# Optimization experiments

Measured on AMD Instinct MI355X. Metric: run time of the kernel, lower is better.

The kernel has to match this reference:

```python
import jax, jax.numpy as jnp
import numpy as np

D_MODEL = 1024
D_STATE = 128
D_CONV = 4
EXPAND = 2
HEADDIM = 64
D_INNER = EXPAND * D_MODEL          # 2048
NHEADS = D_INNER // HEADDIM          # 32
CONV_CH = D_INNER + 2 * D_STATE      # conv acts on x, B, C (ngroups=1)
D_IN_PROJ = 2 * D_INNER + 2 * D_STATE + NHEADS
CHUNK = 128


def setup_inputs() -> dict:
    key = jax.random.key(0)
    ks = jax.random.split(key, 8)
    B, L = 4, 2048
    return {
        'x': jax.random.normal(ks[0], (B, L, D_MODEL), jnp.float32),
        'ln_w': jnp.ones((D_MODEL,), jnp.float32),
        'ln_b': jnp.zeros((D_MODEL,), jnp.float32),
        'in_proj_w': jax.random.normal(ks[1], (D_IN_PROJ, D_MODEL), jnp.float32) * 0.02,
        'conv_w': jax.random.normal(ks[2], (CONV_CH, D_CONV), jnp.float32) * 0.2,
        'conv_b': jnp.zeros((CONV_CH,), jnp.float32),
        'dt_bias': jax.random.normal(ks[3], (NHEADS,), jnp.float32) * 0.5,
        'A_log': jax.random.uniform(ks[4], (NHEADS,), jnp.float32, 0.0, 1.5),
        'D': jax.random.normal(ks[5], (NHEADS,), jnp.float32) * 0.1 + 1.0,
        'norm_w': jnp.ones((D_INNER,), jnp.float32),
        'out_proj_w': jax.random.normal(ks[6], (D_MODEL, D_INNER), jnp.float32) * 0.02,
    }


def segsum(a):
    # a: (..., T) -> (..., T, T) with out[i, j] = sum_{j < k <= i} a[k], -inf above diag
    T = a.shape[-1]
    a_rep = jnp.broadcast_to(a[..., :, None], a.shape + (T,))
    a_masked = jnp.where(jnp.tril(jnp.ones((T, T), bool), -1), a_rep, 0.0)
    seg = jnp.cumsum(a_masked, axis=-2)
    return jnp.where(jnp.tril(jnp.ones((T, T), bool), 0), seg, -jnp.inf)


def _ssd(X, a, Bm, Cm):
    # Chunked SSD (Mamba2). X: (b,l,h,p) pre-multiplied by dt; a: (b,l,h)=dt*A; Bm,Cm: (b,l,n)
    b, l, h, p = X.shape
    c = l // CHUNK
    Xc = X.reshape(b, c, CHUNK, h, p)
    Bc = Bm.reshape(b, c, CHUNK, -1)
    Cc = Cm.reshape(b, c, CHUNK, -1)
    ac = a.reshape(b, c, CHUNK, h).transpose(0, 3, 1, 2)   # (b,h,c,q)
    a_cs = jnp.cumsum(ac, axis=-1)                          # (b,h,c,q)
    Lm = jnp.exp(segsum(ac))                                # (b,h,c,q,q)
    # intra-chunk (diagonal) part
    Y_diag = jnp.einsum('bcln,bcsn,bhcls,bcshp->bclhp', Cc, Bc, Lm, Xc)
    # chunk final states
    decay_states = jnp.exp(a_cs[..., -1:] - a_cs)           # (b,h,c,q)
    states = jnp.einsum('bcln,bhcl,bclhp->bchpn', Bc, decay_states, Xc)
    states = jnp.concatenate([jnp.zeros_like(states[:, :1]), states], axis=1)  # (b,c+1,h,p,n)
    a_chunk = jnp.pad(a_cs[..., -1], ((0, 0), (0, 0), (1, 0)))  # (b,h,c+1)
    decay_chunk = jnp.exp(segsum(a_chunk))                  # (b,h,c+1,c+1)
    prev_states = jnp.einsum('bhzc,bchpn->bzhpn', decay_chunk, states)[:, :-1]  # (b,c,h,p,n)
    # inter-chunk (off-diagonal) part
    Y_off = jnp.einsum('bcln,bchpn,bhcl->bclhp', Cc, prev_states, jnp.exp(a_cs))
    return (Y_diag + Y_off).reshape(b, l, h, p)


def reference(x, ln_w, ln_b, in_proj_w, conv_w, conv_b, dt_bias, A_log, D, norm_w, out_proj_w):
    B, L, _ = x.shape
    # pre-LayerNorm
    mu = x.mean(-1, keepdims=True)
    var = ((x - mu) ** 2).mean(-1, keepdims=True)
    h = (x - mu) / jnp.sqrt(var + 1e-5) * ln_w + ln_b
    # Mamba2 in_proj -> [z, xBC, dt]
    zxbcdt = h @ in_proj_w.T
    z = zxbcdt[..., :D_INNER]
    xBC = zxbcdt[..., D_INNER:D_INNER + CONV_CH]
    dt = jax.nn.softplus(zxbcdt[..., -NHEADS:] + dt_bias)  # (B,L,H)
    # causal depthwise conv1d + SiLU
    xp = jnp.pad(xBC, ((0, 0), (D_CONV - 1, 0), (0, 0)))
    conv = sum(xp[:, k:k + L, :] * conv_w[:, k] for k in range(D_CONV)) + conv_b
    xBC = jax.nn.silu(conv)
    xs = xBC[..., :D_INNER].reshape(B, L, NHEADS, HEADDIM)
    Bm = xBC[..., D_INNER:D_INNER + D_STATE]
    Cm = xBC[..., D_INNER + D_STATE:]
    A = -jnp.exp(A_log)                                    # (H,)
    Y = _ssd(xs * dt[..., None], dt * A, Bm, Cm)
    Y = Y + D[None, None, :, None] * xs                    # D skip connection
    y = Y.reshape(B, L, D_INNER)
    # gated RMSNorm (norm_before_gate=False)
    y = y * jax.nn.silu(z)
    y = y * jax.lax.rsqrt(jnp.mean(y * y, -1, keepdims=True) + 1e-5) * norm_w
    out = y @ out_proj_w.T
    # dropout in eval mode = identity; residual
    return out + x
```

## Files before the change

### kernel.cpp

```cpp
#include <hip/hip_runtime.h>
#include <math.h>

#define BATCH   4
#define LSEQ    2048
#define DMODEL  1024
#define DSTATE  128
#define HEADDIM 64
#define DINNER  2048
#define NHEADS  32
#define CONVCH  2304
#define DINPROJ 4384
#define NPAD    4608
#define CHUNKL  128
#define NCHUNK  16
#define ROWS    (BATCH*LSEQ)

#define B_Z     ((size_t)0)
#define B_XBC   (B_Z   + (size_t)ROWS*DINNER*2)
#define B_DT    (B_XBC + (size_t)ROWS*CONVCH*2)
#define B_XS    (B_DT  + (size_t)ROWS*NHEADS*4)
#define B_BC    (B_XS  + (size_t)ROWS*DINNER*2)
#define B_Y     (B_BC  + (size_t)ROWS*256*2)
#define B_ASUM  (B_Y   + (size_t)ROWS*DINNER*2)
#define B_END   (B_ASUM + (size_t)BATCH*NCHUNK*NHEADS*4)

typedef __attribute__((ext_vector_type(8))) short bf16x8;
typedef __attribute__((ext_vector_type(4))) float f32x4;

__device__ __forceinline__ float b2f(ushort u) {
  union { uint32_t i; float f; } v; v.i = ((uint32_t)u) << 16; return v.f;
}
__device__ __forceinline__ ushort f2b(float f) {
  union { float f; uint32_t i; } v; v.f = f;
  uint32_t r = (v.i + 0x7FFFu + ((v.i >> 16) & 1u)) >> 16;
  return (ushort)r;
}

__device__ __forceinline__ void async_ld16(const void* g, void* l) {
  __builtin_amdgcn_global_load_lds(
      (const __attribute__((address_space(1))) unsigned int*)g,
      (__attribute__((address_space(3))) unsigned int*)l, 16, 0, 0);
}


template<int K>
__device__ __forceinline__ void stage256(const ushort* __restrict__ A,
    const ushort* __restrict__ W, int m0, int n0, int tid, int t,
    ushort* lA, ushort* lB)
{
  const int k0 = t * 64;
  #pragma unroll
  for (int it = 0; it < 4; it++) {
    int s = it*512 + tid;
    int row = s >> 3;
    int g = (s & 7) ^ (row & 7);
    async_ld16(A + (size_t)(m0 + row)*K + k0 + g*8, lA + (size_t)s*8);
  }
  #pragma unroll
  for (int it = 0; it < 4; it++) {
    int s = it*512 + tid;
    int row = s >> 3;
    int g = (s & 7) ^ (row & 7);
    async_ld16(W + (size_t)(n0 + row)*K + k0 + g*8, lB + (size_t)s*8);
  }
}

__device__ __forceinline__ void compute256(const ushort* lA, const ushort* lB,
    int wr, int wc, int rl, int q, f32x4 acc[8][4])
{
  #pragma unroll
  for (int kh = 0; kh < 2; kh++) {
    bf16x8 af[8], bfr[4];
    #pragma unroll
    for (int i = 0; i < 8; i++) {
      int row = wr*128 + i*16 + rl;
      af[i] = *(const bf16x8*)&lA[(size_t)(row*8 + ((kh*4 + q) ^ (row & 7)))*8];
    }
    #pragma unroll
    for (int j = 0; j < 4; j++) {
      int row = wc*64 + j*16 + rl;
      bfr[j] = *(const bf16x8*)&lB[(size_t)(row*8 + ((kh*4 + q) ^ (row & 7)))*8];
    }
    #pragma unroll
    for (int i = 0; i < 8; i++)
      #pragma unroll
      for (int j = 0; j < 4; j++)
        acc[i][j] = __builtin_amdgcn_mfma_f32_16x16x32_bf16(af[i], bfr[j], acc[i][j], 0, 0, 0);
  }
}

template<int K>
__device__ __forceinline__ void stage_tile(const ushort* __restrict__ A,
    const ushort* __restrict__ W, int m0, int n0, int tid, int t,
    ushort* lA, ushort* lB)
{
  const int k0 = t * 64;
  #pragma unroll
  for (int it = 0; it < 4; it++) {
    int s = it*512 + tid;
    int row = s >> 3;
    int g = (s & 7) ^ (row & 7);
    async_ld16(A + (size_t)(m0 + row)*K + k0 + g*8, lA + (size_t)s*8);
  }
  #pragma unroll
  for (int it = 0; it < 2; it++) {
    int s = it*512 + tid;
    int row = s >> 3;
    int g = (s & 7) ^ (row & 7);
    async_ld16(W + (size_t)(n0 + row)*K + k0 + g*8, lB + (size_t)s*8);
  }
}

__device__ __forceinline__ void compute_tile(const ushort* lA, const ushort* lB,
    int wr, int wc, int rl, int q, f32x4 acc[4][4])
{
  #pragma unroll
  for (int kh = 0; kh < 2; kh++) {
    bf16x8 af[4], bfr[4];
    #pragma unroll
    for (int i = 0; i < 4; i++) {
      int row = wr*64 + i*16 + rl;
      af[i] = *(const bf16x8*)&lA[(size_t)(row*8 + ((kh*4 + q) ^ (row & 7)))*8];
    }
    #pragma unroll
    for (int j = 0; j < 4; j++) {
      int row = wc*64 + j*16 + rl;
      bfr[j] = *(const bf16x8*)&lB[(size_t)(row*8 + ((kh*4 + q) ^ (row & 7)))*8];
    }
    #pragma unroll
    for (int i = 0; i < 4; i++)
      #pragma unroll
      for (int j = 0; j < 4; j++)
        acc[i][j] = __builtin_amdgcn_mfma_f32_16x16x32_bf16(af[i], bfr[j], acc[i][j], 0, 0, 0);
  }
}

__global__ __launch_bounds__(256) void convert_win_kernel(const float* __restrict__ W,
                                                          ushort* __restrict__ Wb)
{
  size_t i = (size_t)blockIdx.x*256 + threadIdx.x;
  Wb[i] = (i < (size_t)DINPROJ*DMODEL) ? f2b(W[i]) : (ushort)0;
}

__global__ __launch_bounds__(256) void convert_wout_kernel(const float* __restrict__ W,
                                                           ushort* __restrict__ Wb)
{
  size_t i = (size_t)blockIdx.x*256 + threadIdx.x;
  Wb[i] = f2b(W[i]);
}

__global__ __launch_bounds__(256) void ln_kernel(const float* __restrict__ x,
    const float* __restrict__ w, const float* __restrict__ bias, ushort* __restrict__ h)
{
  const int row = blockIdx.x;
  const int t = threadIdx.x;
  const float* xr = x + (size_t)row * DMODEL;
  float v[4];
  float s = 0.f;
  #pragma unroll
  for (int i = 0; i < 4; i++) { v[i] = xr[t + i*256]; s += v[i]; }
  __shared__ float red[4];
  #pragma unroll
  for (int o = 32; o > 0; o >>= 1) s += __shfl_down(s, o, 64);
  if ((t & 63) == 0) red[t >> 6] = s;
  __syncthreads();
  float mean = (red[0]+red[1]+red[2]+red[3]) * (1.f/DMODEL);
  float vs = 0.f;
  #pragma unroll
  for (int i = 0; i < 4; i++) { float d = v[i]-mean; vs += d*d; }
  #pragma unroll
  for (int o = 32; o > 0; o >>= 1) vs += __shfl_down(vs, o, 64);
  __syncthreads();
  if ((t & 63) == 0) red[t >> 6] = vs;
  __syncthreads();
  float rstd = rsqrtf((red[0]+red[1]+red[2]+red[3]) * (1.f/DMODEL) + 1e-5f);
  ushort* hr = h + (size_t)row * DMODEL;
  #pragma unroll
  for (int i = 0; i < 4; i++) {
    int c = t + i*256;
    hr[c] = f2b((v[i]-mean)*rstd*w[c] + bias[c]);
  }
}

__global__ __launch_bounds__(512, 1) void gemm_inproj_256(const ushort* __restrict__ A,
    const ushort* __restrict__ W, ushort* __restrict__ z, ushort* __restrict__ xbc,
    float* __restrict__ dtr, const float* __restrict__ dtb)
{
  __shared__ ushort smem[65536];
  const int tid = threadIdx.x;
  const int lane = tid & 63;
  const int w = tid >> 6;
  const int wr = w >> 2;
  const int wc = w & 3;
  const int rl = lane & 15;
  const int q  = lane >> 4;

  const int orig = blockIdx.x;
  const int xcd  = orig & 7;
  const int jj   = orig >> 3;
  const int m0 = (xcd*4 + jj/18) * 256;
  const int n0 = (jj % 18) * 256;

  f32x4 acc[8][4];
  #pragma unroll
  for (int i = 0; i < 8; i++)
    #pragma unroll
    for (int j = 0; j < 4; j++) acc[i][j] = (f32x4)(0.f);

  constexpr int NT = DMODEL / 64;
  stage256<DMODEL>(A, W, m0, n0, tid, 0, smem, smem + 16384);
  for (int t = 0; t < NT; t++) {
    const ushort* cA = smem + (t & 1)*32768;
    const ushort* cB = cA + 16384;
    if (t + 1 < NT) {
      ushort* nA = smem + ((t+1) & 1)*32768;
      stage256<DMODEL>(A, W, m0, n0, tid, t + 1, nA, nA + 16384);
      asm volatile("s_waitcnt vmcnt(8)" ::: "memory");
    } else {
      asm volatile("s_waitcnt vmcnt(0)" ::: "memory");
    }
    __builtin_amdgcn_s_barrier();
    __builtin_amdgcn_sched_barrier(0);
    __builtin_amdgcn_s_setprio(1);
    compute256(cA, cB, wr, wc, rl, q, acc);
    __builtin_amdgcn_s_setprio(0);
    __builtin_amdgcn_sched_barrier(0);
    __builtin_amdgcn_s_barrier();
  }

  const int colL = lane & 15;
  const int rowQ = (lane >> 4) * 4;
  if (n0 < DINNER + CONVCH) {
    #pragma unroll
    for (int i = 0; i < 8; i++)
      #pragma unroll
      for (int j = 0; j < 4; j++) {
        int col = wc*64 + j*16 + colL;
        int g = col >> 3;
        #pragma unroll
        for (int r = 0; r < 4; r++) {
          int row = wr*128 + i*16 + rowQ + r;
          int p = (g & 24) | ((g ^ row) & 7);
          smem[row*256 + p*8 + (col & 7)] = f2b(acc[i][j][r]);
        }
      }
    __syncthreads();
    ushort* outp; int coff, ncols;
    if (n0 < DINNER) { outp = z;   coff = n0;          ncols = DINNER; }
    else             { outp = xbc; coff = n0 - DINNER; ncols = CONVCH; }
    #pragma unroll
    for (int it = 0; it < 16; it++) {
      int idx = tid + it*512;
      int row = idx >> 5, g = idx & 31;
      int p = (g & 24) | ((g ^ row) & 7);
      *(uint4*)(outp + (size_t)(m0 + row)*ncols + coff + g*8) =
          *(const uint4*)&smem[row*256 + p*8];
    }
  } else {
    if (wc == 0) {
      #pragma unroll
      for (int i = 0; i < 8; i++)
        #pragma unroll
        for (int j = 0; j < 2; j++) {
          int lc = j*16 + colL;
          float bb = dtb[lc];
          #pragma unroll
          for (int r = 0; r < 4; r++) {
            float v = acc[i][j][r] + bb;
            v = (v > 20.f) ? v : log1pf(expf(v));
            dtr[(size_t)(m0 + wr*128 + i*16 + rowQ + r)*NHEADS + lc] = v;
          }
        }
    }
  }
}

__global__ __launch_bounds__(512, 1) void gemm_outproj_big(const ushort* __restrict__ A,
    const ushort* __restrict__ W, const float* __restrict__ x, float* __restrict__ out)
{
  __shared__ ushort smem[49152];
  ushort* lA0 = smem;
  ushort* lB0 = smem + 32768;
  float* fbuf = (float*)smem;
  const int tid = threadIdx.x;
  const int lane = tid & 63;
  const int w = tid >> 6;
  const int wr = w >> 1;
  const int wc = w & 1;
  const int rl = lane & 15;
  const int q  = lane >> 4;

  const int orig = blockIdx.x;
  const int xcd  = orig & 7;
  const int jj   = orig >> 3;
  const int m0 = (xcd*4 + (jj >> 3)) * 256;
  const int n0 = (jj & 7) * 128;

  f32x4 acc[4][4];
  #pragma unroll
  for (int i = 0; i < 4; i++)
    #pragma unroll
    for (int j = 0; j < 4; j++) acc[i][j] = (f32x4)(0.f);

  constexpr int NT = DINNER / 64;
  stage_tile<DINNER>(A, W, m0, n0, tid, 0, lA0, lB0);
  for (int t = 0; t < NT; t++) {
    const ushort* cA = lA0 + (size_t)(t & 1) * 16384;
    const ushort* cB = lB0 + (size_t)(t & 1) * 8192;
    if (t + 1 < NT) {
      stage_tile<DINNER>(A, W, m0, n0, tid, t + 1,
                         lA0 + (size_t)((t+1) & 1) * 16384,
                         lB0 + (size_t)((t+1) & 1) * 8192);
      asm volatile("s_waitcnt vmcnt(6)" ::: "memory");
    } else {
      asm volatile("s_waitcnt vmcnt(0)" ::: "memory");
    }
    __builtin_amdgcn_s_barrier();
    __builtin_amdgcn_sched_barrier(0);
    __builtin_amdgcn_s_setprio(1);
    compute_tile(cA, cB, wr, wc, rl, q, acc);
    __builtin_amdgcn_s_setprio(0);
    __builtin_amdgcn_sched_barrier(0);
    __builtin_amdgcn_s_barrier();
  }

  const int colL = lane & 15;
  const int rowQ = (lane >> 4) * 4;
  #pragma unroll
  for (int h = 0; h < 2; h++) {
    __syncthreads();
    if ((wr >> 1) == h) {
      #pragma unroll
      for (int i = 0; i < 4; i++)
        #pragma unroll
        for (int j = 0; j < 4; j++) {
          int col = wc*64 + j*16 + colL;
          int g = col >> 2;
          #pragma unroll
          for (int r = 0; r < 4; r++) {
            int row = (wr & 1)*64 + i*16 + rowQ + r;
            fbuf[row*128 + ((g ^ (row & 7)) << 2) + (col & 3)] = acc[i][j][r];
          }
        }
    }
    __syncthreads();
    #pragma unroll
    for (int it = 0; it < 8; it++) {
      int idx = tid + it*512;
      int row = idx >> 5, c4 = idx & 31;
      int gm = m0 + h*128 + row;
      float4 xv = *(const float4*)(x + (size_t)gm*DMODEL + n0 + c4*4);
      float4 vv = *(const float4*)&fbuf[row*128 + ((c4 ^ (row & 7)) << 2)];
      vv.x += xv.x; vv.y += xv.y; vv.z += xv.z; vv.w += xv.w;
      *(float4*)(out + (size_t)gm*DMODEL + n0 + c4*4) = vv;
    }
  }
}

__global__ __launch_bounds__(256) void conv_tiled(const ushort* __restrict__ xbc,
    const float* __restrict__ cw, const float* __restrict__ cb,
    ushort* __restrict__ xs, ushort* __restrict__ bcb)
{
  __shared__ ushort tile[35*256];
  const int tid = threadIdx.x;
  const int ch0 = blockIdx.x * 256;
  const int row0 = blockIdx.y * 32;
  const int l0 = row0 & (LSEQ-1);
  for (int idx = tid; idx < 35*32; idx += 256) {
    int r = idx >> 5, c16 = idx & 31;
    uint4 v = make_uint4(0,0,0,0);
    if (l0 + r - 3 >= 0)
      v = *(const uint4*)(xbc + (size_t)(row0 + r - 3)*CONVCH + ch0 + c16*8);
    *(uint4*)&tile[r*256 + c16*8] = v;
  }
  __syncthreads();
  const int ch = ch0 + tid;
  const float w0 = cw[ch*4+0], w1 = cw[ch*4+1], w2 = cw[ch*4+2], w3 = cw[ch*4+3];
  const float bias = cb[ch];
  const bool isX = (ch0 < DINNER);
  #pragma unroll 4
  for (int r = 0; r < 32; r++) {
    float acc = bias;
    acc = fmaf(b2f(tile[(r+0)*256 + tid]), w0, acc);
    acc = fmaf(b2f(tile[(r+1)*256 + tid]), w1, acc);
    acc = fmaf(b2f(tile[(r+2)*256 + tid]), w2, acc);
    acc = fmaf(b2f(tile[(r+3)*256 + tid]), w3, acc);
    float v = acc / (1.f + expf(-acc));
    if (isX) xs[(size_t)(row0 + r)*DINNER + ch] = f2b(v);
    else     bcb[(size_t)(row0 + r)*256 + (ch - DINNER)] = f2b(v);
  }
}

__global__ __launch_bounds__(256) void states_mfma(
    const ushort* __restrict__ xs, const ushort* __restrict__ bcb, const float* __restrict__ dt,
    const float* __restrict__ A_log, ushort* __restrict__ S, float* __restrict__ asum)
{
  constexpr int LDP = 136;
  __shared__ ushort lBT[128*LDP];
  __shared__ ushort lXT[64*LDP];
  __shared__ float dts[CHUNKL], acs[CHUNKL];
  __shared__ float wtot;
  const int hh = blockIdx.x, c = blockIdx.y, b = blockIdx.z;
  const int tid = threadIdx.x;
  const int lane = tid & 63;
  const int w = tid >> 6;
  const int rbase = b*LSEQ + c*CHUNKL;
  const size_t sbase = (size_t)((b*NCHUNK + c)*NHEADS + hh) * 8192;

  float pre = 0.f;
  if (tid < 128) {
    float myv = dt[(size_t)(rbase + tid)*NHEADS + hh];
    dts[tid] = myv;
    pre = myv;
    #pragma unroll
    for (int o = 1; o < 64; o <<= 1) {
      float u = __shfl_up(pre, o, 64);
      if ((tid & 63) >= o) pre += u;
    }
    if (tid == 63) wtot = pre;
  }
  #pragma unroll
  for (int it = 0; it < 8; it++) {
    int chunk = tid + it*256;
    int l = chunk >> 4, n8 = chunk & 15;
    ushort tmp[8];
    *(uint4*)tmp = *(const uint4*)(bcb + (size_t)(rbase + l)*256 + n8*8);
    #pragma unroll
    for (int u = 0; u < 8; u++) lBT[(n8*8+u)*LDP + l] = tmp[u];
  }
  __syncthreads();
  float alast_loc = 0.f;
  if (tid < 128) {
    float Aval = -expf(A_log[hh]);
    float a = (pre + ((tid >= 64) ? wtot : 0.f)) * Aval;
    acs[tid] = a;
    if (tid == 127) { asum[(b*NCHUNK + c)*NHEADS + hh] = a; }
  }
  __syncthreads();
  alast_loc = acs[CHUNKL-1];
  #pragma unroll
  for (int it = 0; it < 4; it++) {
    int chunk = tid + it*256;
    int l = chunk >> 3, p8 = (chunk & 7)*8;
    ushort tmp[8];
    *(uint4*)tmp = *(const uint4*)(xs + (size_t)(rbase + l)*DINNER + hh*HEADDIM + p8);
    float wl = dts[l] * expf(alast_loc - acs[l]);
    #pragma unroll
    for (int u = 0; u < 8; u++) lXT[(p8+u)*LDP + l] = f2b(b2f(tmp[u]) * wl);
  }
  __syncthreads();

  const int rl = lane & 15;
  const int kq = (lane >> 4) * 8;
  const int nb = w * 32;
  f32x4 acc[4][2];
  #pragma unroll
  for (int i = 0; i < 4; i++) { acc[i][0] = (f32x4)(0.f); acc[i][1] = (f32x4)(0.f); }
  #pragma unroll
  for (int k0 = 0; k0 < 128; k0 += 32) {
    bf16x8 af[4], bfr[2];
    #pragma unroll
    for (int i = 0; i < 4; i++) af[i]  = *(const bf16x8*)&lXT[(i*16 + rl)*LDP + k0 + kq];
    #pragma unroll
    for (int j = 0; j < 2; j++) bfr[j] = *(const bf16x8*)&lBT[(nb + j*16 + rl)*LDP + k0 + kq];
    #pragma unroll
    for (int i = 0; i < 4; i++)
      #pragma unroll
      for (int j = 0; j < 2; j++)
        acc[i][j] = __builtin_amdgcn_mfma_f32_16x16x32_bf16(af[i], bfr[j], acc[i][j], 0, 0, 0);
  }
  __syncthreads();
  const int colL = lane & 15;
  const int rowQ = (lane >> 4) * 4;
  #pragma unroll
  for (int i = 0; i < 4; i++)
    #pragma unroll
    for (int j = 0; j < 2; j++)
      #pragma unroll
      for (int r = 0; r < 4; r++)
        lXT[(i*16 + rowQ + r)*LDP + nb + j*16 + colL] = f2b(acc[i][j][r]);
  __syncthreads();
  #pragma unroll
  for (int it = 0; it < 4; it++) {
    int idx = tid + it*256;
    int row = idx >> 4, c8 = idx & 15;
    *(uint4*)(S + sbase + row*128 + c8*8) = *(const uint4*)&lXT[row*LDP + c8*8];
  }
}

__global__ __launch_bounds__(256) void scan_kernel(ushort* __restrict__ S, const float* __restrict__ asum)
{
  const int hh = blockIdx.x, sl = blockIdx.y, b = blockIdx.z;
  const int base0 = sl*2048 + threadIdx.x;
  float carry[8];
  #pragma unroll
  for (int i = 0; i < 8; i++) carry[i] = 0.f;
  for (int c = 0; c < NCHUNK; c++) {
    ushort* Sp = S + (size_t)((b*NCHUNK + c)*NHEADS + hh) * 8192;
    float dec = expf(asum[(b*NCHUNK + c)*NHEADS + hh]);
    #pragma unroll
    for (int i = 0; i < 8; i++) {
      int idx = base0 + i*256;
      float sv = b2f(Sp[idx]);
      Sp[idx] = f2b(carry[i]);
      carry[i] = fmaf(dec, carry[i], sv);
    }
  }
}

__global__ __launch_bounds__(256) void yssd_mfma(
    const ushort* __restrict__ xs, const ushort* __restrict__ bcb, const float* __restrict__ dt,
    const float* __restrict__ A_log, const float* __restrict__ Dvec,
    const ushort* __restrict__ S, ushort* __restrict__ y)
{
  constexpr int LDP = 136;
  __shared__ ushort lM [128*LDP];
  __shared__ ushort lXT[64*LDP];
  __shared__ float dts[CHUNKL], acs[CHUNKL];
  __shared__ float wtot;
  const int hh = blockIdx.x, c = blockIdx.y, b = blockIdx.z;
  const int tid = threadIdx.x;
  const int lane = tid & 63;
  const int w = tid >> 6;
  const int rbase = b*LSEQ + c*CHUNKL;
  const size_t sbase = (size_t)((b*NCHUNK + c)*NHEADS + hh) * 8192;
  const ushort* Bg = bcb + (size_t)rbase*256;
  const ushort* Cg = Bg + 128;

  #pragma unroll
  for (int it = 0; it < 4; it++) {
    int chunk = tid + it*256;
    int s = chunk >> 3, p0 = (chunk & 7)*8;
    ushort tmp[8];
    *(uint4*)tmp = *(const uint4*)(xs + (size_t)(rbase + s)*DINNER + hh*HEADDIM + p0);
    #pragma unroll
    for (int u = 0; u < 8; u++) lXT[(p0+u)*LDP + s] = tmp[u];
  }
  float pre = 0.f;
  if (tid < 128) {
    float myv = dt[(size_t)(rbase + tid)*NHEADS + hh];
    dts[tid] = myv;
    pre = myv;
    #pragma unroll
    for (int o = 1; o < 64; o <<= 1) {
      float u = __shfl_up(pre, o, 64);
      if ((tid & 63) >= o) pre += u;
    }
    if (tid == 63) wtot = pre;
  }
  __syncthreads();
  if (tid < 128) {
    float Aval = -expf(A_log[hh]);
    acs[tid] = (pre + ((tid >= 64) ? wtot : 0.f)) * Aval;
  }

  const int rl = lane & 15;
  const int kq = (lane >> 4) * 8;
  const int colL = lane & 15;
  const int rowQ = (lane >> 4) * 4;

  const int wm = (w & 1) * 64;
  const int wn = (w >> 1) * 64;
  f32x4 G[4][4];
  #pragma unroll
  for (int i = 0; i < 4; i++)
    #pragma unroll
    for (int j = 0; j < 4; j++) G[i][j] = (f32x4)(0.f);
  #pragma unroll
  for (int k0 = 0; k0 < 128; k0 += 32) {
    bf16x8 af[4], bfr[4];
    #pragma unroll
    for (int i = 0; i < 4; i++) af[i]  = *(const bf16x8*)(Cg + (size_t)(wm + i*16 + rl)*256 + k0 + kq);
    #pragma unroll
    for (int j = 0; j < 4; j++) bfr[j] = *(const bf16x8*)(Bg + (size_t)(wn + j*16 + rl)*256 + k0 + kq);
    #pragma unroll
    for (int i = 0; i < 4; i++)
      #pragma unroll
      for (int j = 0; j < 4; j++)
        G[i][j] = __builtin_amdgcn_mfma_f32_16x16x32_bf16(af[i], bfr[j], G[i][j], 0, 0, 0);
  }
  __syncthreads();

  #pragma unroll
  for (int j = 0; j < 4; j++) {
    int sIdx = wn + j*16 + colL;
    float as = acs[sIdx];
    float ds = dts[sIdx];
    #pragma unroll
    for (int i = 0; i < 4; i++) {
      #pragma unroll
      for (int r = 0; r < 4; r++) {
        int lIdx = wm + i*16 + rowQ + r;
        float m = (lIdx >= sIdx) ? G[i][j][r] * expf(acs[lIdx] - as) * ds : 0.f;
        lM[lIdx*LDP + sIdx] = f2b(m);
      }
    }
  }

  const int om = w * 32;
  f32x4 Y[2][4];
  #pragma unroll
  for (int i = 0; i < 2; i++)
    #pragma unroll
    for (int j = 0; j < 4; j++) Y[i][j] = (f32x4)(0.f);
  #pragma unroll
  for (int k0 = 0; k0 < 128; k0 += 32) {
    bf16x8 a2[2], b2[4];
    #pragma unroll
    for (int i = 0; i < 2; i++) a2[i] = *(const bf16x8*)(Cg + (size_t)(om + i*16 + rl)*256 + k0 + kq);
    #pragma unroll
    for (int j = 0; j < 4; j++) b2[j] = *(const bf16x8*)(S + sbase + (size_t)(j*16 + rl)*128 + k0 + kq);
    #pragma unroll
    for (int i = 0; i < 2; i++)
      #pragma unroll
      for (int j = 0; j < 4; j++)
        Y[i][j] = __builtin_amdgcn_mfma_f32_16x16x32_bf16(a2[i], b2[j], Y[i][j], 0, 0, 0);
  }
  #pragma unroll
  for (int i = 0; i < 2; i++)
    #pragma unroll
    for (int r = 0; r < 4; r++) {
      float e = expf(acs[om + i*16 + rowQ + r]);
      #pragma unroll
      for (int j = 0; j < 4; j++) Y[i][j][r] *= e;
    }
  __syncthreads();

  #pragma unroll
  for (int k0 = 0; k0 < 128; k0 += 32) {
    bf16x8 a3[2], b3[4];
    #pragma unroll
    for (int i = 0; i < 2; i++) a3[i] = *(const bf16x8*)&lM[(om + i*16 + rl)*LDP + k0 + kq];
    #pragma unroll
    for (int j = 0; j < 4; j++) b3[j] = *(const bf16x8*)&lXT[(j*16 + rl)*LDP + k0 + kq];
    #pragma unroll
    for (int i = 0; i < 2; i++)
      #pragma unroll
      for (int j = 0; j < 4; j++)
        Y[i][j] = __builtin_amdgcn_mfma_f32_16x16x32_bf16(a3[i], b3[j], Y[i][j], 0, 0, 0);
  }

  const float Dh = Dvec[hh];
  #pragma unroll
  for (int i = 0; i < 2; i++) {
    #pragma unroll
    for (int r = 0; r < 4; r++) {
      int lIdx = om + i*16 + rowQ + r;
      ushort* yrow = y + (size_t)(rbase + lIdx)*DINNER + hh*HEADDIM;
      #pragma unroll
      for (int j = 0; j < 4; j++) {
        int p = j*16 + colL;
        float val = Y[i][j][r] + Dh * b2f(lXT[p*LDP + lIdx]);
        yrow[p] = f2b(val);
      }
    }
  }
}

__global__ __launch_bounds__(256) void rmsnorm_kernel(ushort* __restrict__ y,
    const ushort* __restrict__ z, const float* __restrict__ nw)
{
  const int row = blockIdx.x;
  const int t = threadIdx.x;
  ushort* yr = y + (size_t)row*DINNER;
  const ushort* zr = z + (size_t)row*DINNER;
  float v[8];
  float ss = 0.f;
  #pragma unroll
  for (int i = 0; i < 8; i++) {
    int c = t + i*256;
    float zz = b2f(zr[c]);
    float g = b2f(yr[c]) * (zz / (1.f + expf(-zz)));
    v[i] = g;
    ss += g*g;
  }
  #pragma unroll
  for (int o = 32; o > 0; o >>= 1) ss += __shfl_down(ss, o, 64);
  __shared__ float red[4];
  if ((t & 63) == 0) red[t >> 6] = ss;
  __syncthreads();
  float scale = rsqrtf((red[0]+red[1]+red[2]+red[3]) * (1.f/DINNER) + 1e-5f);
  #pragma unroll
  for (int i = 0; i < 8; i++) {
    int c = t + i*256;
    yr[c] = f2b(v[i]*scale*nw[c]);
  }
}

extern "C" void kernel_launch(void* const* d_in, const int* in_sizes, int n_in,
                              void* d_out, int out_size, void* d_ws, size_t ws_size,
                              hipStream_t stream)
{
  const float* x    = (const float*)d_in[0];
  const float* lnw  = (const float*)d_in[1];
  const float* lnb  = (const float*)d_in[2];
  const float* win  = (const float*)d_in[3];
  const float* cw   = (const float*)d_in[4];
  const float* cb   = (const float*)d_in[5];
  const float* dtb  = (const float*)d_in[6];
  const float* alog = (const float*)d_in[7];
  const float* dvec = (const float*)d_in[8];
  const float* nw   = (const float*)d_in[9];
  const float* wout = (const float*)d_in[10];
  float* out = (float*)d_out;
  char* ws = (char*)d_ws;
  (void)in_sizes; (void)n_in; (void)out_size;

  if (ws_size < B_END) return;

  ushort* zb   = (ushort*)(ws + B_Z);
  ushort* xbcb = (ushort*)(ws + B_XBC);
  float*  dtr  = (float*) (ws + B_DT);
  ushort* xsb  = (ushort*)(ws + B_XS);
  ushort* bcb  = (ushort*)(ws + B_BC);
  ushort* yb   = (ushort*)(ws + B_Y);
  float*  asum = (float*) (ws + B_ASUM);
  ushort* Sb   = xbcb;
  ushort* hb   = yb;
  ushort* winB = (ushort*)(ws + B_Y + (size_t)ROWS*DMODEL*2);
  ushort* woutB= (ushort*)(ws + B_XBC + (size_t)BATCH*NCHUNK*NHEADS*HEADDIM*DSTATE*2);

  hipLaunchKernelGGL(convert_win_kernel, dim3((NPAD*DMODEL)/256), dim3(256), 0, stream, win, winB);
  hipLaunchKernelGGL(ln_kernel, dim3(ROWS), dim3(256), 0, stream, x, lnw, lnb, hb);
  hipLaunchKernelGGL(gemm_inproj_256, dim3(576), dim3(512), 0, stream, hb, winB, zb, xbcb, dtr, dtb);
  hipLaunchKernelGGL(conv_tiled, dim3(9, ROWS/32), dim3(256), 0, stream, xbcb, cw, cb, xsb, bcb);
  hipLaunchKernelGGL(convert_wout_kernel, dim3((DMODEL*DINNER)/256), dim3(256), 0, stream, wout, woutB);
  hipLaunchKernelGGL(states_mfma, dim3(NHEADS, NCHUNK, BATCH), dim3(256), 0, stream,
                     xsb, bcb, dtr, alog, Sb, asum);
  hipLaunchKernelGGL(scan_kernel, dim3(NHEADS, 4, BATCH), dim3(256), 0, stream, Sb, asum);
  hipLaunchKernelGGL(yssd_mfma, dim3(NHEADS, NCHUNK, BATCH), dim3(256), 0, stream,
                     xsb, bcb, dtr, alog, dvec, Sb, yb);
  hipLaunchKernelGGL(rmsnorm_kernel, dim3(ROWS), dim3(256), 0, stream, yb, zb, nw);
  hipLaunchKernelGGL(gemm_outproj_big, dim3(256), dim3(512), 0, stream, yb, woutB, x, out);
}
```

Baseline: 473.3 us.

## Restructure in_proj GEMM into quadrant phases with finer-grained async staging

The in_proj 256x256 GEMM main loop is rewritten so each K-step is split into four quadrant phases (2x2 sub-tiles of 128x128), each with its own barrier and MFMA burst. Half-tile global-to-LDS loads are interleaved between phases, with explicit vmcnt waits, so memory traffic overlaps compute at finer granularity than whole-tile double buffering. The warp layout changes to 2x4 with per-quadrant accumulators, and A fragments are reused across the two N quadrants. It adds more barriers per K-step, and the hand-tuned vmcnt counts risk races if they are wrong.

```diff
diff --git a/kernel.cpp b/kernel.cpp
--- a/kernel.cpp
+++ b/kernel.cpp
@@ -42,9 +42,61 @@
       (__attribute__((address_space(3))) unsigned int*)l, 16, 0, 0);
 }
 
+#define VMG(n) asm volatile("s_waitcnt vmcnt(" #n ")" ::: "memory")
+
 
 template<int K>
-__device__ __forceinline__ void stage256(const ushort* __restrict__ A,
+__device__ __forceinline__ void stage_half(const ushort* __restrict__ M,
+    int row0, int k0, int tid, ushort* dst)
+{
+  #pragma unroll
+  for (int it = 0; it < 2; it++) {
+    int s = it*512 + tid;
+    int rl = s >> 3;
+    int g = (s & 7) ^ (rl & 7);
+    async_ld16(M + (size_t)(row0 + rl)*K + k0 + g*8, dst + (size_t)s*8);
+  }
+}
+
+template<int QM, int QN, bool RDA>
+__device__ __forceinline__ void qphase(const ushort* __restrict__ bA,
+    const ushort* __restrict__ bB, int wq, int wn, int rl, int q,
+    bf16x8 (&af)[2][4], bf16x8 (&bfr)[2][2], f32x4 (&acc)[2][2][4][2])
+{
+  __builtin_amdgcn_s_barrier();
+  __builtin_amdgcn_sched_barrier(0);
+  if (RDA) {
+    #pragma unroll
+    for (int kh = 0; kh < 2; kh++)
+      #pragma unroll
+      for (int ii = 0; ii < 4; ii++) {
+        int row = QM*128 + wq*64 + ii*16 + rl;
+        af[kh][ii] = *(const bf16x8*)&bA[(size_t)(row*8 + ((kh*4 + q) ^ (row & 7)))*8];
+      }
+  }
+  #pragma unroll
+  for (int kh = 0; kh < 2; kh++)
+    #pragma unroll
+    for (int jj = 0; jj < 2; jj++) {
+      int row = QN*128 + wn*32 + jj*16 + rl;
+      bfr[kh][jj] = *(const bf16x8*)&bB[(size_t)(row*8 + ((kh*4 + q) ^ (row & 7)))*8];
+    }
+  __builtin_amdgcn_s_setprio(1);
+  #pragma unroll
+  for (int kh = 0; kh < 2; kh++)
+    #pragma unroll
+    for (int ii = 0; ii < 4; ii++)
+      #pragma unroll
+      for (int jj = 0; jj < 2; jj++)
+        acc[QM][QN][ii][jj] = __builtin_amdgcn_mfma_f32_16x16x32_bf16(
+            af[kh][ii], bfr[kh][jj], acc[QM][QN][ii][jj], 0, 0, 0);
+  __builtin_amdgcn_s_setprio(0);
+  __builtin_amdgcn_sched_barrier(0);
+  __builtin_amdgcn_s_barrier();
+}
+
+template<int K>
+__device__ __forceinline__ void stage_tile(const ushort* __restrict__ A,
     const ushort* __restrict__ W, int m0, int n0, int tid, int t,
     ushort* lA, ushort* lB)
 {
@@ -57,52 +109,6 @@
     async_ld16(A + (size_t)(m0 + row)*K + k0 + g*8, lA + (size_t)s*8);
   }
   #pragma unroll
-  for (int it = 0; it < 4; it++) {
-    int s = it*512 + tid;
-    int row = s >> 3;
-    int g = (s & 7) ^ (row & 7);
-    async_ld16(W + (size_t)(n0 + row)*K + k0 + g*8, lB + (size_t)s*8);
-  }
-}
-
-__device__ __forceinline__ void compute256(const ushort* lA, const ushort* lB,
-    int wr, int wc, int rl, int q, f32x4 acc[8][4])
-{
-  #pragma unroll
-  for (int kh = 0; kh < 2; kh++) {
-    bf16x8 af[8], bfr[4];
-    #pragma unroll
-    for (int i = 0; i < 8; i++) {
-      int row = wr*128 + i*16 + rl;
-      af[i] = *(const bf16x8*)&lA[(size_t)(row*8 + ((kh*4 + q) ^ (row & 7)))*8];
-    }
-    #pragma unroll
-    for (int j = 0; j < 4; j++) {
-      int row = wc*64 + j*16 + rl;
-      bfr[j] = *(const bf16x8*)&lB[(size_t)(row*8 + ((kh*4 + q) ^ (row & 7)))*8];
-    }
-    #pragma unroll
-    for (int i = 0; i < 8; i++)
-      #pragma unroll
-      for (int j = 0; j < 4; j++)
-        acc[i][j] = __builtin_amdgcn_mfma_f32_16x16x32_bf16(af[i], bfr[j], acc[i][j], 0, 0, 0);
-  }
-}
-
-template<int K>
-__device__ __forceinline__ void stage_tile(const ushort* __restrict__ A,
-    const ushort* __restrict__ W, int m0, int n0, int tid, int t,
-    ushort* lA, ushort* lB)
-{
-  const int k0 = t * 64;
-  #pragma unroll
-  for (int it = 0; it < 4; it++) {
-    int s = it*512 + tid;
-    int row = s >> 3;
-    int g = (s & 7) ^ (row & 7);
-    async_ld16(A + (size_t)(m0 + row)*K + k0 + g*8, lA + (size_t)s*8);
-  }
-  #pragma unroll
   for (int it = 0; it < 2; it++) {
     int s = it*512 + tid;
     int row = s >> 3;
@@ -182,7 +188,7 @@
   }
 }
 
-__global__ __launch_bounds__(512, 1) void gemm_inproj_256(const ushort* __restrict__ A,
+__global__ __launch_bounds__(512, 1) void gemm_inproj_8ph(const ushort* __restrict__ A,
     const ushort* __restrict__ W, ushort* __restrict__ z, ushort* __restrict__ xbc,
     float* __restrict__ dtr, const float* __restrict__ dtb)
 {
@@ -190,60 +196,112 @@
   const int tid = threadIdx.x;
   const int lane = tid & 63;
   const int w = tid >> 6;
-  const int wr = w >> 2;
-  const int wc = w & 3;
+  const int wq = w >> 2;
+  const int wn = w & 3;
   const int rl = lane & 15;
   const int q  = lane >> 4;
 
   const int orig = blockIdx.x;
   const int xcd  = orig & 7;
-  const int jj   = orig >> 3;
-  const int m0 = (xcd*4 + jj/18) * 256;
-  const int n0 = (jj % 18) * 256;
-
-  f32x4 acc[8][4];
-  #pragma unroll
-  for (int i = 0; i < 8; i++)
-    #pragma unroll
-    for (int j = 0; j < 4; j++) acc[i][j] = (f32x4)(0.f);
-
+  const int jj_  = orig >> 3;
+  const int m0 = (xcd*4 + jj_/18) * 256;
+  const int n0 = (jj_ % 18) * 256;
+
+  f32x4 acc[2][2][4][2];
+  #pragma unroll
+  for (int a = 0; a < 2; a++)
+    #pragma unroll
+    for (int b = 0; b < 2; b++)
+      #pragma unroll
+      for (int c = 0; c < 4; c++)
+        #pragma unroll
+        for (int d = 0; d < 2; d++) acc[a][b][c][d] = (f32x4)(0.f);
+
+  bf16x8 af[2][4], bfr[2][2];
   constexpr int NT = DMODEL / 64;
-  stage256<DMODEL>(A, W, m0, n0, tid, 0, smem, smem + 16384);
-  for (int t = 0; t < NT; t++) {
-    const ushort* cA = smem + (t & 1)*32768;
-    const ushort* cB = cA + 16384;
-    if (t + 1 < NT) {
-      ushort* nA = smem + ((t+1) & 1)*32768;
-      stage256<DMODEL>(A, W, m0, n0, tid, t + 1, nA, nA + 16384);
-      asm volatile("s_waitcnt vmcnt(8)" ::: "memory");
-    } else {
-      asm volatile("s_waitcnt vmcnt(0)" ::: "memory");
-    }
-    __builtin_amdgcn_s_barrier();
-    __builtin_amdgcn_sched_barrier(0);
-    __builtin_amdgcn_s_setprio(1);
-    compute256(cA, cB, wr, wc, rl, q, acc);
-    __builtin_amdgcn_s_setprio(0);
-    __builtin_amdgcn_sched_barrier(0);
-    __builtin_amdgcn_s_barrier();
+
+  {
+    ushort* A0 = smem;            ushort* B0 = smem + 16384;
+    ushort* A1 = smem + 32768;    ushort* B1 = A1 + 16384;
+    stage_half<DMODEL>(A, m0+0,   0,  tid, A0);
+    stage_half<DMODEL>(W, n0+0,   0,  tid, B0);
+    stage_half<DMODEL>(W, n0+128, 0,  tid, B0 + 8192);
+    stage_half<DMODEL>(A, m0+128, 0,  tid, A0 + 8192);
+    stage_half<DMODEL>(A, m0+0,   64, tid, A1);
+    stage_half<DMODEL>(W, n0+0,   64, tid, B1);
+  }
+
+  for (int t = 0; t < NT-2; t++) {
+    const int d = t & 1;
+    const ushort* bA = smem + d*32768;
+    const ushort* bB = bA + 16384;
+    ushort* nA = smem + (d^1)*32768;
+    ushort* nB = nA + 16384;
+    ushort* sA = smem + d*32768;
+    ushort* sB = sA + 16384;
+    stage_half<DMODEL>(W, n0+128, (t+1)*64, tid, nB + 8192);
+    VMG(10);
+    qphase<0,0,true >(bA, bB, wq, wn, rl, q, af, bfr, acc);
+    stage_half<DMODEL>(A, m0+128, (t+1)*64, tid, nA + 8192);
+    VMG(10);
+    qphase<0,1,false>(bA, bB, wq, wn, rl, q, af, bfr, acc);
+    stage_half<DMODEL>(A, m0+0, (t+2)*64, tid, sA);
+    VMG(10);
+    qphase<1,0,true >(bA, bB, wq, wn, rl, q, af, bfr, acc);
+    stage_half<DMODEL>(W, n0+0, (t+2)*64, tid, sB);
+    qphase<1,1,false>(bA, bB, wq, wn, rl, q, af, bfr, acc);
+  }
+  {
+    const int t = NT-2;
+    const int d = t & 1;
+    const ushort* bA = smem + d*32768;
+    const ushort* bB = bA + 16384;
+    ushort* nA = smem + (d^1)*32768;
+    ushort* nB = nA + 16384;
+    stage_half<DMODEL>(W, n0+128, (t+1)*64, tid, nB + 8192);
+    VMG(10);
+    qphase<0,0,true >(bA, bB, wq, wn, rl, q, af, bfr, acc);
+    stage_half<DMODEL>(A, m0+128, (t+1)*64, tid, nA + 8192);
+    VMG(10);
+    qphase<0,1,false>(bA, bB, wq, wn, rl, q, af, bfr, acc);
+    VMG(8);
+    qphase<1,0,true >(bA, bB, wq, wn, rl, q, af, bfr, acc);
+    qphase<1,1,false>(bA, bB, wq, wn, rl, q, af, bfr, acc);
+  }
+  {
+    const int t = NT-1;
+    const int d = t & 1;
+    const ushort* bA = smem + d*32768;
+    const ushort* bB = bA + 16384;
+    VMG(4);
+    qphase<0,0,true >(bA, bB, wq, wn, rl, q, af, bfr, acc);
+    VMG(2);
+    qphase<0,1,false>(bA, bB, wq, wn, rl, q, af, bfr, acc);
+    VMG(0);
+    qphase<1,0,true >(bA, bB, wq, wn, rl, q, af, bfr, acc);
+    qphase<1,1,false>(bA, bB, wq, wn, rl, q, af, bfr, acc);
   }
 
   const int colL = lane & 15;
   const int rowQ = (lane >> 4) * 4;
   if (n0 < DINNER + CONVCH) {
     #pragma unroll
-    for (int i = 0; i < 8; i++)
-      #pragma unroll
-      for (int j = 0; j < 4; j++) {
-        int col = wc*64 + j*16 + colL;
-        int g = col >> 3;
+    for (int qm = 0; qm < 2; qm++)
+      #pragma unroll
+      for (int qn = 0; qn < 2; qn++)
         #pragma unroll
-        for (int r = 0; r < 4; r++) {
-          int row = wr*128 + i*16 + rowQ + r;
-          int p = (g & 24) | ((g ^ row) & 7);
-          smem[row*256 + p*8 + (col & 7)] = f2b(acc[i][j][r]);
-        }
-      }
+        for (int ii = 0; ii < 4; ii++)
+          #pragma unroll
+          for (int jj = 0; jj < 2; jj++) {
+            int col = qn*128 + wn*32 + jj*16 + colL;
+            int g = col >> 3;
+            #pragma unroll
+            for (int r = 0; r < 4; r++) {
+              int row = qm*128 + wq*64 + ii*16 + rowQ + r;
+              int p = (g & 24) | ((g ^ row) & 7);
+              smem[row*256 + p*8 + (col & 7)] = f2b(acc[qm][qn][ii][jj][r]);
+            }
+          }
     __syncthreads();
     ushort* outp; int coff, ncols;
     if (n0 < DINNER) { outp = z;   coff = n0;          ncols = DINNER; }
@@ -257,20 +315,22 @@
           *(const uint4*)&smem[row*256 + p*8];
     }
   } else {
-    if (wc == 0) {
-      #pragma unroll
-      for (int i = 0; i < 8; i++)
+    if (wn == 0) {
+      #pragma unroll
+      for (int qm = 0; qm < 2; qm++)
         #pragma unroll
-        for (int j = 0; j < 2; j++) {
-          int lc = j*16 + colL;
-          float bb = dtb[lc];
+        for (int ii = 0; ii < 4; ii++)
           #pragma unroll
-          for (int r = 0; r < 4; r++) {
-            float v = acc[i][j][r] + bb;
-            v = (v > 20.f) ? v : log1pf(expf(v));
-            dtr[(size_t)(m0 + wr*128 + i*16 + rowQ + r)*NHEADS + lc] = v;
+          for (int jj = 0; jj < 2; jj++) {
+            int lc = jj*16 + colL;
+            float bb = dtb[lc];
+            #pragma unroll
+            for (int r = 0; r < 4; r++) {
+              float v = acc[qm][0][ii][jj][r] + bb;
+              v = (v > 20.f) ? v : log1pf(expf(v));
+              dtr[(size_t)(m0 + qm*128 + wq*64 + ii*16 + rowQ + r)*NHEADS + lc] = v;
+            }
           }
-        }
     }
   }
 }
@@ -722,7 +782,7 @@
 
   hipLaunchKernelGGL(convert_win_kernel, dim3((NPAD*DMODEL)/256), dim3(256), 0, stream, win, winB);
   hipLaunchKernelGGL(ln_kernel, dim3(ROWS), dim3(256), 0, stream, x, lnw, lnb, hb);
-  hipLaunchKernelGGL(gemm_inproj_256, dim3(576), dim3(512), 0, stream, hb, winB, zb, xbcb, dtr, dtb);
+  hipLaunchKernelGGL(gemm_inproj_8ph, dim3(576), dim3(512), 0, stream, hb, winB, zb, xbcb, dtr, dtb);
   hipLaunchKernelGGL(conv_tiled, dim3(9, ROWS/32), dim3(256), 0, stream, xbcb, cw, cb, xsb, bcb);
   hipLaunchKernelGGL(convert_wout_kernel, dim3((DMODEL*DINNER)/256), dim3(256), 0, stream, wout, woutB);
   hipLaunchKernelGGL(states_mfma, dim3(NHEADS, NCHUNK, BATCH), dim3(256), 0, stream,
```

Result: no change. 476.2 us (+0.6%).
